# Optimization experiments

Hardware: AMD Instinct MI355X
Metric: run time of the kernel (lower is better)

## Reference

```python
import jax, jax.numpy as jnp
import numpy as np

N_HEAD = 16


def setup_inputs() -> dict:
    key = jax.random.key(0)
    k1, k2, k3 = jax.random.split(key, 3)
    B, T, C = 4, 2048, 1024
    x = jax.random.normal(k1, (B, T, C), dtype=jnp.float32)
    # Dense kernels (no bias), scaled like glorot-ish init
    W_attn = jax.random.normal(k2, (C, 3 * C), dtype=jnp.float32) * (1.0 / np.sqrt(C))
    W_proj = jax.random.normal(k3, (C, C), dtype=jnp.float32) * (1.0 / np.sqrt(C))
    return {"x": x, "W_attn": W_attn, "W_proj": W_proj}


def reference(x, W_attn, W_proj):
    # Vanilla causal multi-head self-attention (dropout is identity at inference).
    B, T, C = x.shape
    H = N_HEAD
    hs = C // H
    qkv = x @ W_attn                       # (B, T, 3C)
    q, k, v = jnp.split(qkv, 3, axis=-1)
    q = q.reshape(B, T, H, hs)             # (B, T, H, hs)
    k = k.reshape(B, T, H, hs)
    v = v.reshape(B, T, H, hs)
    scale = 1.0 / jnp.sqrt(jnp.asarray(hs, dtype=x.dtype))
    att = jnp.einsum('bthd,bshd->bhts', q, k) * scale   # (B, H, T, T)
    causal = jnp.tril(jnp.ones((T, T), dtype=bool))
    att = jnp.where(causal[None, None], att, -jnp.inf)
    att = jax.nn.softmax(att, axis=-1)
    y = jnp.einsum('bhts,bshd->bthd', att, v)            # (B, T, H, hs)
    y = y.reshape(B, T, C)
    return y @ W_proj
```

## Files before the change

### kernel.cpp

```cpp
#include <hip/hip_runtime.h>
#include <hip/hip_bf16.h>
#include <cstdint>
#include <cstddef>


typedef unsigned short ushort_t;
typedef __attribute__((ext_vector_type(8))) short short8;
typedef __attribute__((ext_vector_type(4))) float f32x4;
typedef __attribute__((ext_vector_type(16))) float f32x16;

#define AS1 __attribute__((address_space(1)))
#define AS3 __attribute__((address_space(3)))

#if __has_builtin(__builtin_amdgcn_exp2f)
#define EXP2(x) __builtin_amdgcn_exp2f(x)
#else
#define EXP2(x) exp2f(x)
#endif

__device__ __forceinline__ ushort_t f2bf(float f) {
  union { float f; unsigned u; } c; c.f = f;
  unsigned u = c.u;
  return (ushort_t)((u + 0x7FFFu + ((u >> 16) & 1u)) >> 16);
}

__device__ __forceinline__ unsigned cvt_pk_bf16(float a, float b) {
  unsigned r;
  asm("v_cvt_pk_bf16_f32 %0, %1, %2" : "=v"(r) : "v"(a), "v"(b));
  return r;
}

__global__ __launch_bounds__(256) void k_f32_to_bf16(const float* __restrict__ in,
                                                     ushort_t* __restrict__ out) {
  const size_t i = ((size_t)blockIdx.x * 256 + threadIdx.x) * 8;
  f32x4 a = *(const f32x4*)(in + i);
  f32x4 b = *(const f32x4*)(in + i + 4);
  short8 o;
  o[0] = (short)f2bf(a[0]); o[1] = (short)f2bf(a[1]);
  o[2] = (short)f2bf(a[2]); o[3] = (short)f2bf(a[3]);
  o[4] = (short)f2bf(b[0]); o[5] = (short)f2bf(b[1]);
  o[6] = (short)f2bf(b[2]); o[7] = (short)f2bf(b[3]);
  *(short8*)(out + i) = o;
}

__global__ __launch_bounds__(256) void k_transpose_bf16(const float* __restrict__ in,
                                                        ushort_t* __restrict__ out,
                                                        int R, int C) {
  __shared__ float tile[32][33];
  const int tx = threadIdx.x & 31, ty = threadIdx.x >> 5;
  const int c0 = blockIdx.x * 32, r0 = blockIdx.y * 32;
#pragma unroll
  for (int i = 0; i < 32; i += 8)
    tile[ty + i][tx] = in[(size_t)(r0 + ty + i) * C + c0 + tx];
  __syncthreads();
#pragma unroll
  for (int i = 0; i < 32; i += 8)
    out[(size_t)(c0 + ty + i) * R + r0 + tx] = f2bf(tile[tx][ty + i]);
}

__global__ __launch_bounds__(256) void k_vt(const ushort_t* __restrict__ qkv,
                                            ushort_t* __restrict__ vt) {
  __shared__ ushort_t tl[64][72];
  const int T = 2048, C3 = 3072;
  const int t0 = blockIdx.x * 64, h = blockIdx.y, b = blockIdx.z;
  const int r = threadIdx.x >> 4;
  const int c4 = (threadIdx.x & 15) * 4;
  const ushort_t* src = qkv + (size_t)(b * T + t0) * C3 + 2048 + h * 64;
#pragma unroll
  for (int p = 0; p < 4; p++) {
    const int row = p * 16 + r;
    *(short4*)&tl[row][c4] = *(const short4*)(src + (size_t)row * C3 + c4);
  }
  __syncthreads();
  ushort_t* dst = vt + (size_t)((b * 16 + h) * 64) * T + t0;
#pragma unroll
  for (int p = 0; p < 4; p++) {
    const int d = p * 16 + r;
    short4 o;
    o.x = (short)tl[c4 + 0][d];
    o.y = (short)tl[c4 + 1][d];
    o.z = (short)tl[c4 + 2][d];
    o.w = (short)tl[c4 + 3][d];
    *(short4*)(dst + (size_t)d * T + c4) = o;
  }
}

template <int OUTMODE>
__global__ __launch_bounds__(256) void k_gemm_bt(const ushort_t* __restrict__ A,
                                                 const ushort_t* __restrict__ Bt,
                                                 void* __restrict__ Cout,
                                                 ushort_t* __restrict__ vtout,
                                                 int N, int K) {
  __shared__ ushort_t As[128 * 64];
  __shared__ ushort_t Bs[128 * 64];
  const int tid = threadIdx.x;
  const int wave = tid >> 6, lane = tid & 63;
  const int c = lane & 15, g = lane >> 4;
  const int wm = wave >> 1, wn = wave & 1;

  const int nwg = gridDim.x * gridDim.y;
  int wg = blockIdx.y * gridDim.x + blockIdx.x;
  {
    const int qd = nwg >> 3, rm = nwg & 7;
    const int xcd = wg & 7, idx = wg >> 3;
    wg = (xcd < rm ? xcd * (qd + 1) : rm * (qd + 1) + (xcd - rm) * qd) + idx;
  }
  const int bx = wg % gridDim.x, by = wg / gridDim.x;

  f32x4 acc[4][4];
#pragma unroll
  for (int m = 0; m < 4; m++)
#pragma unroll
    for (int n = 0; n < 4; n++) acc[m][n] = (f32x4){0.f, 0.f, 0.f, 0.f};

  for (int k0 = 0; k0 < K; k0 += 64) {
#pragma unroll
    for (int i = 0; i < 4; i++) {
      const int flat = i * 256 + tid;
      const ushort_t* srcA = A + (size_t)(by * 128 + (flat >> 3)) * K + k0 + (flat & 7) * 8;
      const ushort_t* srcB = Bt + (size_t)(bx * 128 + (flat >> 3)) * K + k0 + (flat & 7) * 8;
      const int ldsoff = (i * 256 + wave * 64) * 16;
      __builtin_amdgcn_global_load_lds((const AS1 void*)srcA,
                                       (AS3 void*)((char*)As + ldsoff), 16, 0, 0);
      __builtin_amdgcn_global_load_lds((const AS1 void*)srcB,
                                       (AS3 void*)((char*)Bs + ldsoff), 16, 0, 0);
    }
    __syncthreads();
#pragma unroll
    for (int kk = 0; kk < 2; kk++) {
      short8 af[4], bfr[4];
#pragma unroll
      for (int m = 0; m < 4; m++)
        af[m] = *(const short8*)(As + (wm * 64 + m * 16 + c) * 64 + kk * 32 + g * 8);
#pragma unroll
      for (int n = 0; n < 4; n++)
        bfr[n] = *(const short8*)(Bs + (wn * 64 + n * 16 + c) * 64 + kk * 32 + g * 8);
#pragma unroll
      for (int m = 0; m < 4; m++)
#pragma unroll
        for (int n = 0; n < 4; n++)
          acc[m][n] = __builtin_amdgcn_mfma_f32_16x16x32_bf16(af[m], bfr[n], acc[m][n], 0, 0, 0);
    }
    __syncthreads();
  }

  if (OUTMODE == 2 && bx >= 16) {
#pragma unroll
    for (int m = 0; m < 4; m++)
#pragma unroll
      for (int n = 0; n < 4; n++) {
        const int cv = bx * 128 + wn * 64 + n * 16 + c - 2048;
        const int hh = cv >> 6, d = cv & 63;
        const int row = by * 128 + wm * 64 + m * 16 + g * 4;
        const int bb = row >> 11, t = row & 2047;
        short4 o;
        o.x = (short)f2bf(acc[m][n][0]);
        o.y = (short)f2bf(acc[m][n][1]);
        o.z = (short)f2bf(acc[m][n][2]);
        o.w = (short)f2bf(acc[m][n][3]);
        *(short4*)(vtout + ((size_t)((bb * 16 + hh) * 64 + d)) * 2048 + t) = o;
      }
    return;
  }

#pragma unroll
  for (int m = 0; m < 4; m++)
#pragma unroll
    for (int n = 0; n < 4; n++) {
      const int col = bx * 128 + wn * 64 + n * 16 + c;
#pragma unroll
      for (int r = 0; r < 4; r++) {
        const int row = by * 128 + wm * 64 + m * 16 + g * 4 + r;
        if (OUTMODE != 0)
          ((ushort_t*)Cout)[(size_t)row * N + col] = f2bf(acc[m][n][r]);
        else
          ((float*)Cout)[(size_t)row * N + col] = acc[m][n][r];
      }
    }
}


__device__ __forceinline__ void stage_kv(const ushort_t* __restrict__ Kp,
                                         const ushort_t* __restrict__ Vt,
                                         ushort_t* Kl, ushort_t* Vl,
                                         int kb, int wave, int lane) {
  const int C3 = 3072, T = 2048;
#pragma unroll
  for (int j = 0; j < 2; j++) {
    const int rbase = wave * 16 + j * 8;
    const int r = rbase + (lane >> 3);
    const int cbg = ((lane & 7) ^ (r & 7)) << 4;
    const int ldsbase = rbase * 128;
    __builtin_amdgcn_global_load_lds(
        (const AS1 void*)(Kp + (size_t)(kb + r) * C3 + (cbg >> 1)),
        (AS3 void*)((char*)Kl + ldsbase), 16, 0, 0);
    __builtin_amdgcn_global_load_lds(
        (const AS1 void*)(Vt + (size_t)r * T + kb + (cbg >> 1)),
        (AS3 void*)((char*)Vl + ldsbase), 16, 0, 0);
  }
}

__global__ __launch_bounds__(256, 2) void k_attn(const ushort_t* __restrict__ qkv,
                                                 const ushort_t* __restrict__ vt,
                                                 ushort_t* __restrict__ y) {
  const int T = 2048, C3 = 3072, Cc = 1024;
  __shared__ ushort_t Kl[2][64 * 64];
  __shared__ ushort_t Vl[2][64 * 64];

  const int tid = threadIdx.x;
  const int wave = tid >> 6, lane = tid & 63;
  const int l31 = lane & 31, hi = lane >> 5;
  const bool hib = (hi != 0);
  const int swr = (l31 & 7) << 4;
  const int b = blockIdx.z, h = blockIdx.y;
  const int tmap = ((int)blockIdx.x + ((b >> 1) << 3)) & 15;
  const int qi = (b & 1) ? (15 - tmap) : tmap;
  const int qbase = qi * 128 + wave * 32;
  const int q = qbase + l31;

  const size_t base = (size_t)b * T * C3 + h * 64;
  const ushort_t* Q = qkv + base;
  const ushort_t* Kp = qkv + base + 1024;
  const ushort_t* Vt = vt + (size_t)((b * 16 + h) * 64) * T;

  const float KS = 0.125f * 1.44269504f;
  const float THR = 8.0f;

  short8 qfr[4];
  {
    const ushort_t* qp = Q + (size_t)q * C3 + 8 * hi;
#pragma unroll
    for (int i = 0; i < 4; i++) qfr[i] = *(const short8*)(qp + 16 * i);
  }

  f32x16 yacc0 = (f32x16)(0.0f), yacc1 = (f32x16)(0.0f);
  float mx = -3.0e38f, ssum = 0.f;

  const int nk_blk = (qi + 1) * 128;
  stage_kv(Kp, Vt, Kl[0], Vl[0], 0, wave, lane);
  __syncthreads();
  int cur = 0;

  for (int kb = 0; kb < nk_blk; kb += 64) {
    if (kb + 64 < nk_blk)
      stage_kv(Kp, Vt, Kl[cur ^ 1], Vl[cur ^ 1], kb + 64, wave, lane);

    if (kb < qbase + 32) {
      const char* Kbuf = (const char*)Kl[cur];
      const char* Vbuf = (const char*)Vl[cur];

      f32x16 s0 = (f32x16)(0.0f), s1 = (f32x16)(0.0f);
#pragma unroll
      for (int i = 0; i < 4; i++) {
        const int colb = (32 * i + 16 * hi) ^ swr;
        const short8 ka0 = *(const short8*)(Kbuf + l31 * 128 + colb);
        const short8 ka1 = *(const short8*)(Kbuf + (32 + l31) * 128 + colb);
        s0 = __builtin_amdgcn_mfma_f32_32x32x16_bf16(ka0, qfr[i], s0, 0, 0, 0);
        s1 = __builtin_amdgcn_mfma_f32_32x32x16_bf16(ka1, qfr[i], s1, 0, 0, 0);
      }

      if (kb + 63 > qbase) {
#pragma unroll
        for (int r = 0; r < 16; r++) {
          const int key = kb + (r & 3) + 8 * (r >> 2) + 4 * hi;
          if (key > q) s0[r] = -1.0e30f;
          if (key + 32 > q) s1[r] = -1.0e30f;
        }
      }

      float t16[16];
#pragma unroll
      for (int r = 0; r < 16; r++) t16[r] = fmaxf(s0[r], s1[r]);
#pragma unroll
      for (int r = 0; r < 8; r++) t16[r] = fmaxf(t16[r], t16[r + 8]);
#pragma unroll
      for (int r = 0; r < 4; r++) t16[r] = fmaxf(t16[r], t16[r + 4]);
      float tm = fmaxf(fmaxf(t16[0], t16[1]), fmaxf(t16[2], t16[3]));
      tm = fmaxf(tm, __shfl_xor(tm, 32));
      const float cand = tm * KS;

      if (__any(cand > mx + THR)) {
        const float mnew = fmaxf(mx, cand);
        const float alpha = EXP2(mx - mnew);
        ssum *= alpha;
#pragma unroll
        for (int r = 0; r < 16; r++) { yacc0[r] *= alpha; yacc1[r] *= alpha; }
        mx = mnew;
      }

#pragma unroll
      for (int r = 0; r < 16; r++) {
        s0[r] = EXP2(__builtin_fmaf(s0[r], KS, -mx));
        s1[r] = EXP2(__builtin_fmaf(s1[r], KS, -mx));
      }
      {
        float ss[16];
#pragma unroll
        for (int r = 0; r < 16; r++) ss[r] = s0[r] + s1[r];
#pragma unroll
        for (int r = 0; r < 8; r++) ss[r] += ss[r + 8];
#pragma unroll
        for (int r = 0; r < 4; r++) ss[r] += ss[r + 4];
        float ts = (ss[0] + ss[1]) + (ss[2] + ss[3]);
        ts += __shfl_xor(ts, 32);
        ssum += ts;
      }

      union U4 { unsigned u[4]; short8 v; };
      U4 pb[4];
      {
        unsigned dw[4][4];
#pragma unroll
        for (int j = 0; j < 2; j++) {
          dw[j][0] = cvt_pk_bf16(s0[j * 8 + 0], s0[j * 8 + 1]);
          dw[j][1] = cvt_pk_bf16(s0[j * 8 + 2], s0[j * 8 + 3]);
          dw[j][2] = cvt_pk_bf16(s0[j * 8 + 4], s0[j * 8 + 5]);
          dw[j][3] = cvt_pk_bf16(s0[j * 8 + 6], s0[j * 8 + 7]);
          dw[2 + j][0] = cvt_pk_bf16(s1[j * 8 + 0], s1[j * 8 + 1]);
          dw[2 + j][1] = cvt_pk_bf16(s1[j * 8 + 2], s1[j * 8 + 3]);
          dw[2 + j][2] = cvt_pk_bf16(s1[j * 8 + 4], s1[j * 8 + 5]);
          dw[2 + j][3] = cvt_pk_bf16(s1[j * 8 + 6], s1[j * 8 + 7]);
        }
#pragma unroll
        for (int j = 0; j < 4; j++) {
          const unsigned d0 = dw[j][0], d1 = dw[j][1], d2 = dw[j][2], d3 = dw[j][3];
          const unsigned snd0 = hib ? d0 : d2;
          const unsigned snd1 = hib ? d1 : d3;
          const unsigned rcv0 = (unsigned)__shfl_xor((int)snd0, 32);
          const unsigned rcv1 = (unsigned)__shfl_xor((int)snd1, 32);
          pb[j].u[0] = hib ? rcv0 : d0;
          pb[j].u[1] = hib ? rcv1 : d1;
          pb[j].u[2] = hib ? d2 : rcv0;
          pb[j].u[3] = hib ? d3 : rcv1;
        }
      }

#pragma unroll
      for (int sj = 0; sj < 4; sj++) {
        const int colb = (sj * 32 + 16 * hi) ^ swr;
        const short8 va0 = *(const short8*)(Vbuf + l31 * 128 + colb);
        const short8 va1 = *(const short8*)(Vbuf + (32 + l31) * 128 + colb);
        yacc0 = __builtin_amdgcn_mfma_f32_32x32x16_bf16(va0, pb[sj].v, yacc0, 0, 0, 0);
        yacc1 = __builtin_amdgcn_mfma_f32_32x32x16_bf16(va1, pb[sj].v, yacc1, 0, 0, 0);
      }
    }

    __syncthreads();
    cur ^= 1;
  }

  const float inv = 1.0f / ssum;
  ushort_t* yp = y + (size_t)(b * T + q) * Cc + h * 64;
#pragma unroll
  for (int gi = 0; gi < 4; gi++) {
    short4 o0, o1;
    o0.x = (short)f2bf(yacc0[gi * 4 + 0] * inv);
    o0.y = (short)f2bf(yacc0[gi * 4 + 1] * inv);
    o0.z = (short)f2bf(yacc0[gi * 4 + 2] * inv);
    o0.w = (short)f2bf(yacc0[gi * 4 + 3] * inv);
    o1.x = (short)f2bf(yacc1[gi * 4 + 0] * inv);
    o1.y = (short)f2bf(yacc1[gi * 4 + 1] * inv);
    o1.z = (short)f2bf(yacc1[gi * 4 + 2] * inv);
    o1.w = (short)f2bf(yacc1[gi * 4 + 3] * inv);
    *(short4*)(yp + 8 * gi + 4 * hi) = o0;
    *(short4*)(yp + 32 + 8 * gi + 4 * hi) = o1;
  }
}

extern "C" void kernel_launch(void* const* d_in, const int* in_sizes, int n_in,
                              void* d_out, int out_size, void* d_ws, size_t ws_size,
                              hipStream_t stream) {
  const float* x = (const float*)d_in[0];
  const float* Wat = (const float*)d_in[1];
  const float* Wpr = (const float*)d_in[2];
  float* out = (float*)d_out;

  const int T = 2048, B = 4, H = 16, Cc = 1024;
  const int M = B * T;

  char* ws = (char*)d_ws;
  const size_t MB = 1024 * 1024;
  ushort_t* xb = (ushort_t*)ws;
  ushort_t* wat = (ushort_t*)(ws + 16 * MB);
  ushort_t* wpt = (ushort_t*)(ws + 24 * MB);
  ushort_t* qkv = (ushort_t*)(ws + 32 * MB);
  ushort_t* yb = (ushort_t*)(ws + 80 * MB);

  const bool big_ws = (ws_size >= (size_t)112 * MB);

  k_f32_to_bf16<<<dim3((M * Cc) / (8 * 256)), 256, 0, stream>>>(x, xb);
  k_transpose_bf16<<<dim3(3072 / 32, 1024 / 32), 256, 0, stream>>>(Wat, wat, 1024, 3072);
  k_transpose_bf16<<<dim3(1024 / 32, 1024 / 32), 256, 0, stream>>>(Wpr, wpt, 1024, 1024);

  if (big_ws) {
    ushort_t* vtb = (ushort_t*)(ws + 96 * MB);
    k_gemm_bt<2><<<dim3(3072 / 128, M / 128), 256, 0, stream>>>(xb, wat, qkv, vtb, 3072, 1024);
    k_attn<<<dim3(16, H, B), 256, 0, stream>>>(qkv, vtb, yb);
  } else {
    ushort_t* vtb = xb;
    k_gemm_bt<1><<<dim3(3072 / 128, M / 128), 256, 0, stream>>>(xb, wat, qkv, nullptr, 3072, 1024);
    k_vt<<<dim3(T / 64, H, B), 256, 0, stream>>>(qkv, vtb);
    k_attn<<<dim3(16, H, B), 256, 0, stream>>>(qkv, vtb, yb);
  }

  k_gemm_bt<0><<<dim3(1024 / 128, M / 128), 256, 0, stream>>>(yb, wpt, out, nullptr, 1024, 1024);
}
```

Before: 196.3 us.

## Replace GEMM with 256x128 tile, 8-wave, triple-buffered swizzled LDS pipeline

Replaces the 128x128 single-buffered GEMM kernel, used for both the QKV and output projections, with a 256x128 tile run by 512 threads. Global-to-LDS loads go into a three-stage ring buffer with prefetch two tiles ahead. LDS columns are XOR-swizzled to avoid bank conflicts, and MFMA phases are wrapped in raised wave priority and explicit barriers. The aim is to hide global load latency and raise data reuse, at the cost of more LDS use, fewer workgroups, and fragile hand-placed waitcnt counts.

```diff
diff --git a/kernel.cpp b/kernel.cpp
--- a/kernel.cpp
+++ b/kernel.cpp
@@ -85,18 +85,31 @@
   }
 }
 
+__device__ __forceinline__ void stage_unit(const ushort_t* __restrict__ X, int K,
+                                           char* ldsbase, int tid, int w) {
+#pragma unroll
+  for (int j = 0; j < 2; j++) {
+    const int rl = j * 64 + (tid >> 3);
+    const int gc = ((tid & 7) ^ (rl & 7)) << 3;
+    __builtin_amdgcn_global_load_lds(
+        (const AS1 void*)(X + (size_t)rl * K + gc),
+        (AS3 void*)(ldsbase + (j * 64 + w * 8) * 128), 16, 0, 0);
+  }
+}
+
 template <int OUTMODE>
-__global__ __launch_bounds__(256) void k_gemm_bt(const ushort_t* __restrict__ A,
-                                                 const ushort_t* __restrict__ Bt,
-                                                 void* __restrict__ Cout,
-                                                 ushort_t* __restrict__ vtout,
-                                                 int N, int K) {
-  __shared__ ushort_t As[128 * 64];
-  __shared__ ushort_t Bs[128 * 64];
+__global__ __launch_bounds__(512, 2) void k_gemm256(const ushort_t* __restrict__ A,
+                                                    const ushort_t* __restrict__ Bt,
+                                                    void* __restrict__ Cout,
+                                                    ushort_t* __restrict__ vtout,
+                                                    int N, int K) {
+  __shared__ ushort_t As[3 * 256 * 64];
+  __shared__ ushort_t Bs[3 * 128 * 64];
+
   const int tid = threadIdx.x;
-  const int wave = tid >> 6, lane = tid & 63;
+  const int w = tid >> 6, lane = tid & 63;
   const int c = lane & 15, g = lane >> 4;
-  const int wm = wave >> 1, wn = wave & 1;
+  const int wr = w >> 1, wc = w & 1;
 
   const int nwg = gridDim.x * gridDim.y;
   int wg = blockIdx.y * gridDim.x + blockIdx.x;
@@ -105,7 +118,20 @@
     const int xcd = wg & 7, idx = wg >> 3;
     wg = (xcd < rm ? xcd * (qd + 1) : rm * (qd + 1) + (xcd - rm) * qd) + idx;
   }
-  const int bx = wg % gridDim.x, by = wg / gridDim.x;
+  const int bxn = wg % gridDim.x, by = wg / gridDim.x;
+
+  const ushort_t* Abase = A + (size_t)(by * 256) * K;
+  const ushort_t* Bbase = Bt + (size_t)(bxn * 128) * K;
+  const int NT = K >> 6;
+
+  auto stageT = [&](int tt) {
+    const int s = tt % 3, k0 = tt * 64;
+    char* Ab = (char*)As + s * 32768;
+    char* Bb = (char*)Bs + s * 16384;
+    stage_unit(Abase + k0, K, Ab, tid, w);
+    stage_unit(Abase + (size_t)128 * K + k0, K, Ab + 16384, tid, w);
+    stage_unit(Bbase + k0, K, Bb, tid, w);
+  };
 
   f32x4 acc[4][4];
 #pragma unroll
@@ -113,52 +139,90 @@
 #pragma unroll
     for (int n = 0; n < 4; n++) acc[m][n] = (f32x4){0.f, 0.f, 0.f, 0.f};
 
-  for (int k0 = 0; k0 < K; k0 += 64) {
-#pragma unroll
-    for (int i = 0; i < 4; i++) {
-      const int flat = i * 256 + tid;
-      const ushort_t* srcA = A + (size_t)(by * 128 + (flat >> 3)) * K + k0 + (flat & 7) * 8;
-      const ushort_t* srcB = Bt + (size_t)(bx * 128 + (flat >> 3)) * K + k0 + (flat & 7) * 8;
-      const int ldsoff = (i * 256 + wave * 64) * 16;
-      __builtin_amdgcn_global_load_lds((const AS1 void*)srcA,
-                                       (AS3 void*)((char*)As + ldsoff), 16, 0, 0);
-      __builtin_amdgcn_global_load_lds((const AS1 void*)srcB,
-                                       (AS3 void*)((char*)Bs + ldsoff), 16, 0, 0);
+  stageT(0);
+  stageT(1);
+  __builtin_amdgcn_sched_barrier(0);
+  asm volatile("s_waitcnt vmcnt(6)" ::: "memory");
+  __builtin_amdgcn_s_barrier();
+  __builtin_amdgcn_sched_barrier(0);
+
+  for (int t = 0; t < NT; ++t) {
+    const int cur = t % 3;
+    const char* Ab = (const char*)As + cur * 32768;
+    const char* Bb = (const char*)Bs + cur * 16384;
+
+    {
+      short8 af[4], bv[4];
+#pragma unroll
+      for (int m = 0; m < 4; m++) {
+        const int r = wr * 64 + m * 16 + c;
+        af[m] = *(const short8*)(Ab + r * 128 + ((g * 16) ^ ((r & 7) << 4)));
+      }
+#pragma unroll
+      for (int n = 0; n < 4; n++) {
+        const int r = wc * 64 + n * 16 + c;
+        bv[n] = *(const short8*)(Bb + r * 128 + ((g * 16) ^ ((r & 7) << 4)));
+      }
+      if (t + 2 < NT) stageT(t + 2);
+      __builtin_amdgcn_s_barrier();
+      __builtin_amdgcn_s_setprio(1);
+#pragma unroll
+      for (int m = 0; m < 4; m++)
+#pragma unroll
+        for (int n = 0; n < 4; n++)
+          acc[m][n] = __builtin_amdgcn_mfma_f32_16x16x32_bf16(af[m], bv[n], acc[m][n], 0, 0, 0);
+      __builtin_amdgcn_s_setprio(0);
+      __builtin_amdgcn_s_barrier();
     }
-    __syncthreads();
-#pragma unroll
-    for (int kk = 0; kk < 2; kk++) {
-      short8 af[4], bfr[4];
+
+    {
+      short8 af[4], bv[4];
+#pragma unroll
+      for (int m = 0; m < 4; m++) {
+        const int r = wr * 64 + m * 16 + c;
+        af[m] = *(const short8*)(Ab + r * 128 + ((64 + g * 16) ^ ((r & 7) << 4)));
+      }
+#pragma unroll
+      for (int n = 0; n < 4; n++) {
+        const int r = wc * 64 + n * 16 + c;
+        bv[n] = *(const short8*)(Bb + r * 128 + ((64 + g * 16) ^ ((r & 7) << 4)));
+      }
+      __builtin_amdgcn_s_barrier();
+      __builtin_amdgcn_s_setprio(1);
 #pragma unroll
       for (int m = 0; m < 4; m++)
-        af[m] = *(const short8*)(As + (wm * 64 + m * 16 + c) * 64 + kk * 32 + g * 8);
-#pragma unroll
-      for (int n = 0; n < 4; n++)
-        bfr[n] = *(const short8*)(Bs + (wn * 64 + n * 16 + c) * 64 + kk * 32 + g * 8);
-#pragma unroll
-      for (int m = 0; m < 4; m++)
 #pragma unroll
         for (int n = 0; n < 4; n++)
-          acc[m][n] = __builtin_amdgcn_mfma_f32_16x16x32_bf16(af[m], bfr[n], acc[m][n], 0, 0, 0);
+          acc[m][n] = __builtin_amdgcn_mfma_f32_16x16x32_bf16(af[m], bv[n], acc[m][n], 0, 0, 0);
+      __builtin_amdgcn_s_setprio(0);
     }
-    __syncthreads();
-  }
-
-  if (OUTMODE == 2 && bx >= 16) {
+
+    if (t + 1 < NT) {
+      __builtin_amdgcn_sched_barrier(0);
+      if (t + 2 < NT)
+        asm volatile("s_waitcnt vmcnt(6)" ::: "memory");
+      else
+        asm volatile("s_waitcnt vmcnt(0)" ::: "memory");
+      __builtin_amdgcn_s_barrier();
+      __builtin_amdgcn_sched_barrier(0);
+    }
+  }
+
+  if (OUTMODE == 2 && bxn >= 16) {
 #pragma unroll
     for (int m = 0; m < 4; m++)
 #pragma unroll
       for (int n = 0; n < 4; n++) {
-        const int cv = bx * 128 + wn * 64 + n * 16 + c - 2048;
+        const int cv = bxn * 128 + wc * 64 + n * 16 + c - 2048;
         const int hh = cv >> 6, d = cv & 63;
-        const int row = by * 128 + wm * 64 + m * 16 + g * 4;
-        const int bb = row >> 11, t = row & 2047;
+        const int row = by * 256 + wr * 64 + m * 16 + g * 4;
+        const int bb = row >> 11, tt = row & 2047;
         short4 o;
         o.x = (short)f2bf(acc[m][n][0]);
         o.y = (short)f2bf(acc[m][n][1]);
         o.z = (short)f2bf(acc[m][n][2]);
         o.w = (short)f2bf(acc[m][n][3]);
-        *(short4*)(vtout + ((size_t)((bb * 16 + hh) * 64 + d)) * 2048 + t) = o;
+        *(short4*)(vtout + ((size_t)((bb * 16 + hh) * 64 + d)) * 2048 + tt) = o;
       }
     return;
   }
@@ -167,10 +231,10 @@
   for (int m = 0; m < 4; m++)
 #pragma unroll
     for (int n = 0; n < 4; n++) {
-      const int col = bx * 128 + wn * 64 + n * 16 + c;
+      const int col = bxn * 128 + wc * 64 + n * 16 + c;
 #pragma unroll
       for (int r = 0; r < 4; r++) {
-        const int row = by * 128 + wm * 64 + m * 16 + g * 4 + r;
+        const int row = by * 256 + wr * 64 + m * 16 + g * 4 + r;
         if (OUTMODE != 0)
           ((ushort_t*)Cout)[(size_t)row * N + col] = f2bf(acc[m][n][r]);
         else
@@ -178,7 +242,6 @@
       }
     }
 }
-
 
 __device__ __forceinline__ void stage_kv(const ushort_t* __restrict__ Kp,
                                          const ushort_t* __restrict__ Vt,
@@ -394,14 +457,14 @@
 
   if (big_ws) {
     ushort_t* vtb = (ushort_t*)(ws + 96 * MB);
-    k_gemm_bt<2><<<dim3(3072 / 128, M / 128), 256, 0, stream>>>(xb, wat, qkv, vtb, 3072, 1024);
+    k_gemm256<2><<<dim3(3072 / 128, M / 256), 512, 0, stream>>>(xb, wat, qkv, vtb, 3072, 1024);
     k_attn<<<dim3(16, H, B), 256, 0, stream>>>(qkv, vtb, yb);
   } else {
     ushort_t* vtb = xb;
-    k_gemm_bt<1><<<dim3(3072 / 128, M / 128), 256, 0, stream>>>(xb, wat, qkv, nullptr, 3072, 1024);
+    k_gemm256<1><<<dim3(3072 / 128, M / 256), 512, 0, stream>>>(xb, wat, qkv, nullptr, 3072, 1024);
     k_vt<<<dim3(T / 64, H, B), 256, 0, stream>>>(qkv, vtb);
     k_attn<<<dim3(16, H, B), 256, 0, stream>>>(qkv, vtb, yb);
   }
 
-  k_gemm_bt<0><<<dim3(1024 / 128, M / 128), 256, 0, stream>>>(yb, wpt, out, nullptr, 1024, 1024);
-}
+  k_gemm256<0><<<dim3(1024 / 128, M / 256), 512, 0, stream>>>(yb, wpt, out, nullptr, 1024, 1024);
+}
```

Result: faster. 182.5 us (-7.0%).
